# Optimization experiments

Measured on AMD Instinct MI355X. Metric: run time of the kernel, lower is better.

Reference implementation:

```python
import jax, jax.numpy as jnp
import numpy as np

B, S, D = 2, 2048, 1024
H, E = 16, 64  # n_head, d_head


def setup_inputs() -> dict:
    key = jax.random.key(0)
    ks = jax.random.split(key, 5)
    scale = 0.02
    return {
        "x": jax.random.normal(ks[0], (B, S, D), dtype=jnp.float32),
        "Wq": jax.random.normal(ks[1], (H, D, E), dtype=jnp.float32) * scale,
        "Wk": jax.random.normal(ks[2], (H, D, E), dtype=jnp.float32) * scale,
        "Wv": jax.random.normal(ks[3], (H, D, E), dtype=jnp.float32) * scale,
        "Wproj": jax.random.normal(ks[4], (D, D), dtype=jnp.float32) * scale,
    }


def reference(x, Wq, Wk, Wv, Wproj):
    # Batched equivalent of the per-head Python loop.
    q = jnp.einsum("bsd,hde->bhse", x, Wq)  # [B,H,S,E]
    k = jnp.einsum("bsd,hde->bhse", x, Wk)
    v = jnp.einsum("bsd,hde->bhse", x, Wv)
    scale = 1.0 / jnp.sqrt(jnp.asarray(E, dtype=x.dtype))
    scores = jnp.einsum("bhse,bhte->bhst", q, k) * scale  # [B,H,S,S]
    causal = jnp.tril(jnp.ones((S, S), dtype=bool))
    scores = jnp.where(causal, scores, jnp.asarray(-jnp.inf, dtype=scores.dtype))
    attn = jax.nn.softmax(scores, axis=-1)
    out = jnp.einsum("bhst,bhte->bhse", attn, v)  # [B,H,S,E]
    # concat heads along last dim (head h -> contiguous slice), then proj
    out = out.transpose(0, 2, 1, 3).reshape(B, S, H * E)
    return out @ Wproj.T  # nn.Linear: y = x W^T
```

## Files before the change

kernel.cpp:

```cpp
#include <hip/hip_runtime.h>
#include <hip/hip_bf16.h>

typedef __attribute__((ext_vector_type(8))) short short8;
typedef __attribute__((ext_vector_type(4))) short s16x4;
typedef __attribute__((ext_vector_type(4))) float f32x4;
typedef __hip_bfloat16 bf16;

#define NB 2
#define NS 2048
#define ND 1024
#define NH 16
#define NE 64

#define QSCALE 0.1803368867f

#define ASYNC16(g, l) __builtin_amdgcn_global_load_lds( \
    (const __attribute__((address_space(1))) void*)(g), \
    (__attribute__((address_space(3))) void*)(l), 16, 0, 0)

__device__ __forceinline__ unsigned short bf16b(float x) {
  __hip_bfloat16 h = __float2bfloat16(x);
  unsigned short u;
  __builtin_memcpy(&u, &h, 2);
  return u;
}

__global__ __launch_bounds__(256) void prep_all(const float* __restrict__ x,
                                                bf16* __restrict__ xb,
                                                const float* __restrict__ wp,
                                                bf16* __restrict__ wpb,
                                                const float* __restrict__ Wq,
                                                const float* __restrict__ Wk,
                                                const float* __restrict__ Wv,
                                                bf16* __restrict__ WT) {
  const int bid = blockIdx.x;
  const int tid = threadIdx.x;
  if (bid < 2560) {
    const float* src;
    bf16* dst;
    int i;
    if (bid < 2048) { src = x;  dst = xb;  i = (bid * 256 + tid) * 8; }
    else            { src = wp; dst = wpb; i = ((bid - 2048) * 256 + tid) * 8; }
    const float4 a = *(const float4*)(src + i);
    const float4 b = *(const float4*)(src + i + 4);
    *(ushort4*)(dst + i)     = make_ushort4(bf16b(a.x), bf16b(a.y), bf16b(a.z), bf16b(a.w));
    *(ushort4*)(dst + i + 4) = make_ushort4(bf16b(b.x), bf16b(b.y), bf16b(b.z), bf16b(b.w));
    return;
  }
  const int tb = bid - 2560;
  const int w = tb >> 8;
  const int xx = tb & 255;
  const float* W = (w == 0) ? Wq : ((w == 1) ? Wk : Wv);
  const int h = xx >> 4, kt = xx & 15;
  __shared__ bf16 tile[64][65];
#pragma unroll
  for (int i = 0; i < 16; ++i) {
    const int idx = i * 256 + tid, kl = idx >> 6, e = idx & 63;
    tile[kl][e] = __float2bfloat16(W[((size_t)h * ND + kt * 64 + kl) * NE + e]);
  }
  __syncthreads();
#pragma unroll
  for (int i = 0; i < 16; ++i) {
    const int idx = i * 256 + tid, el = idx >> 6, kl = idx & 63;
    WT[((size_t)w * NH * NE + h * NE + el) * ND + kt * 64 + kl] = tile[kl][el];
  }
}

__global__ __launch_bounds__(256) void qkv_gemm(const bf16* __restrict__ X,
                                                const bf16* __restrict__ WT,
                                                bf16* __restrict__ Qo,
                                                bf16* __restrict__ Ko,
                                                bf16* __restrict__ Vo) {
  const int w = blockIdx.z;
  const bf16* Bm = WT + (size_t)w * (NH * NE * ND);
  const int n0 = blockIdx.x * 128, m0 = blockIdx.y * 128;
  __shared__ __align__(16) bf16 As[2][128 * 32];
  __shared__ __align__(16) bf16 Bs[2][128 * 32];
  const int tid = threadIdx.x;
  const int lane = tid & 63, wid = tid >> 6;
  const int wm = wid >> 1, wn = wid & 1;
  const int g = lane >> 4, c = lane & 15;
  const int row4 = tid >> 2;
  const int kcs = ((tid & 3) ^ ((tid >> 3) & 3)) * 8;

  auto stage = [&](int buf, int k0) {
    ASYNC16(X + (size_t)(m0 + row4) * ND + k0 + kcs, As[buf] + wid * 512);
    ASYNC16(X + (size_t)(m0 + 64 + row4) * ND + k0 + kcs, As[buf] + 2048 + wid * 512);
    ASYNC16(Bm + (size_t)(n0 + row4) * ND + k0 + kcs, Bs[buf] + wid * 512);
    ASYNC16(Bm + (size_t)(n0 + 64 + row4) * ND + k0 + kcs, Bs[buf] + 2048 + wid * 512);
  };

  f32x4 acc[4][4] = {};
  stage(0, 0);
  __syncthreads();
  int cur = 0;
  for (int k0 = 0; k0 < ND; k0 += 32) {
    if (k0 + 32 < ND) stage(cur ^ 1, k0 + 32);
    const short* as = (const short*)As[cur];
    const short* bs = (const short*)Bs[cur];
    short8 af[4], bq[4];
#pragma unroll
    for (int i = 0; i < 4; ++i)
      af[i] = *(const short8*)&as[(wm * 64 + i * 16 + c) * 32 + ((g ^ ((c >> 1) & 3)) * 8)];
#pragma unroll
    for (int j = 0; j < 4; ++j)
      bq[j] = *(const short8*)&bs[(wn * 64 + j * 16 + c) * 32 + ((g ^ ((c >> 1) & 3)) * 8)];
    __builtin_amdgcn_s_setprio(1);
#pragma unroll
    for (int i = 0; i < 4; ++i)
#pragma unroll
      for (int j = 0; j < 4; ++j)
        acc[i][j] = __builtin_amdgcn_mfma_f32_16x16x32_bf16(af[i], bq[j], acc[i][j], 0, 0, 0);
    __builtin_amdgcn_s_setprio(0);
    __syncthreads();
    cur ^= 1;
  }
  const float osc = (w == 0) ? QSCALE : 1.0f;
#pragma unroll
  for (int i = 0; i < 4; ++i) {
    const int mg0 = m0 + wm * 64 + i * 16 + g * 4;
#pragma unroll
    for (int j = 0; j < 4; ++j) {
      const int ng = n0 + wn * 64 + j * 16 + c;
      const int h = ng >> 6, e = ng & 63;
      if (w == 2) {
        const int b = mg0 >> 11, s = mg0 & 2047;
        ushort4 pk = make_ushort4(bf16b(acc[i][j][0]), bf16b(acc[i][j][1]),
                                  bf16b(acc[i][j][2]), bf16b(acc[i][j][3]));
        *(ushort4*)&Vo[(((size_t)b * NH + h) * NE + e) * NS + s] = pk;
      } else {
        bf16* O = (w == 0) ? Qo : Ko;
#pragma unroll
        for (int r = 0; r < 4; ++r) {
          const int m = mg0 + r, b = m >> 11, s = m & 2047;
          O[(((size_t)b * NH + h) * NS + s) * NE + e] = __float2bfloat16(acc[i][j][r] * osc);
        }
      }
    }
  }
}

__global__ __launch_bounds__(256, 4) void attn_fwd(const bf16* __restrict__ Qb,
                                                   const bf16* __restrict__ Kb,
                                                   const bf16* __restrict__ Vt,
                                                   bf16* __restrict__ AO) {
  const int bh = blockIdx.x;
  const int qi = blockIdx.y;
  const int a = qi & 7, k = qi >> 3;
  const int qt = (k == 0) ? a : (k == 1) ? 31 - a : (k == 2) ? a + 8 : 23 - a;
  const int q0 = qt * 64;
  __shared__ __align__(16) bf16 Ks[2][64 * 64];
  __shared__ __align__(16) bf16 Vs[2][64 * 64];
  __shared__ __align__(16) bf16 Ps[4][16 * 64];
  const int tid = threadIdx.x, lane = tid & 63, wid = tid >> 6;
  const int g = lane >> 4, c = lane & 15;
  const int sw8 = ((tid & 7) ^ ((tid >> 3) & 7)) * 8;
  const bf16* Qg = Qb + (size_t)bh * NS * NE;
  const bf16* Kg = Kb + (size_t)bh * NS * NE;
  const bf16* Vg = Vt + (size_t)bh * NE * NS;

  short8 aq[2];
#pragma unroll
  for (int kk = 0; kk < 2; ++kk)
    aq[kk] = *(const short8*)&Qg[(size_t)(q0 + wid * 16 + c) * NE + kk * 32 + g * 8];

  const short8 bones = {0x3F80, 0x3F80, 0x3F80, 0x3F80, 0x3F80, 0x3F80, 0x3F80, 0x3F80};

  f32x4 acc_o[4] = {};
  f32x4 acc_l = {};
  float mrun = -1.0e30f;

  auto stage = [&](int buf, int t0) {
    ASYNC16(Kg + (size_t)(t0 + (tid >> 3)) * NE + sw8,      Ks[buf] + wid * 512);
    ASYNC16(Kg + (size_t)(t0 + 32 + (tid >> 3)) * NE + sw8, Ks[buf] + 2048 + wid * 512);
    ASYNC16(Vg + (size_t)(tid >> 3) * NS + t0 + sw8,        Vs[buf] + wid * 512);
    ASYNC16(Vg + (size_t)(32 + (tid >> 3)) * NS + t0 + sw8, Vs[buf] + 2048 + wid * 512);
  };

  const int nt = qt + 1;
  int cur = 0;
  stage(0, 0);
  __syncthreads();
  for (int tt = 0; tt < nt; ++tt) {
    const int t0 = tt * 64;
    if (tt + 1 < nt) stage(cur ^ 1, t0 + 64);
    const bool diag = (tt == nt - 1);
    f32x4 sacc[4] = {};
    const short* ks = (const short*)Ks[cur];
    const short* vs = (const short*)Vs[cur];
    __builtin_amdgcn_s_setprio(1);
#pragma unroll
    for (int kk = 0; kk < 2; ++kk) {
      short8 bk[4];
#pragma unroll
      for (int tn = 0; tn < 4; ++tn)
        bk[tn] = *(const short8*)&ks[(tn * 16 + c) * 64 + (((kk * 4 + g) ^ (c & 7)) * 8)];
#pragma unroll
      for (int tn = 0; tn < 4; ++tn)
        sacc[tn] = __builtin_amdgcn_mfma_f32_16x16x32_bf16(bk[tn], aq[kk], sacc[tn], 0, 0, 0);
    }
    __builtin_amdgcn_s_setprio(0);
    float mx = -1.0e30f;
#pragma unroll
    for (int tn = 0; tn < 4; ++tn) {
#pragma unroll
      for (int r = 0; r < 4; ++r) {
        float v = sacc[tn][r];
        if (diag) {
          const int tcol = t0 + tn * 16 + g * 4 + r;
          const int qrow = q0 + wid * 16 + c;
          v = (tcol <= qrow) ? v : -1.0e30f;
          sacc[tn][r] = v;
        }
        mx = fmaxf(mx, v);
      }
    }
    if (__any(mx > mrun + 8.0f)) {
      mx = fmaxf(mx, __shfl_xor(mx, 16));
      mx = fmaxf(mx, __shfl_xor(mx, 32));
      const float mnew = fmaxf(mrun, mx);
      const float alpha = __builtin_exp2f(mrun - mnew);
      mrun = mnew;
      float al[4];
#pragma unroll
      for (int r = 0; r < 4; ++r) al[r] = __shfl(alpha, g * 4 + r);
#pragma unroll
      for (int fe = 0; fe < 4; ++fe)
#pragma unroll
        for (int r = 0; r < 4; ++r) acc_o[fe][r] *= al[r];
#pragma unroll
      for (int r = 0; r < 4; ++r) acc_l[r] *= al[r];
    }
    short* psw = (short*)Ps[wid];
#pragma unroll
    for (int tn = 0; tn < 4; ++tn) {
      s16x4 pw;
#pragma unroll
      for (int r = 0; r < 4; ++r)
        pw[r] = (short)bf16b(__builtin_exp2f(sacc[tn][r] - mrun));
      const int blk = (2 * tn + (g >> 1)) ^ (c & 7);
      *(s16x4*)&psw[c * 64 + blk * 8 + (g & 1) * 4] = pw;
    }
    const short* ps = (const short*)Ps[wid];
    __builtin_amdgcn_s_setprio(1);
#pragma unroll
    for (int ks2 = 0; ks2 < 2; ++ks2) {
      short8 ap, bv[4];
      ap = *(const short8*)&ps[c * 64 + (((ks2 * 4 + g) ^ (c & 7)) * 8)];
      acc_l = __builtin_amdgcn_mfma_f32_16x16x32_bf16(ap, bones, acc_l, 0, 0, 0);
#pragma unroll
      for (int fe = 0; fe < 4; ++fe)
        bv[fe] = *(const short8*)&vs[(fe * 16 + c) * 64 + (((ks2 * 4 + g) ^ (c & 7)) * 8)];
#pragma unroll
      for (int fe = 0; fe < 4; ++fe)
        acc_o[fe] = __builtin_amdgcn_mfma_f32_16x16x32_bf16(ap, bv[fe], acc_o[fe], 0, 0, 0);
    }
    __builtin_amdgcn_s_setprio(0);
    __syncthreads();
    cur ^= 1;
  }
  const int b = bh >> 4, h = bh & 15;
#pragma unroll
  for (int fe = 0; fe < 4; ++fe)
#pragma unroll
    for (int r = 0; r < 4; ++r) {
      const int s = q0 + wid * 16 + g * 4 + r;
      const float val = acc_o[fe][r] / acc_l[r];
      AO[((size_t)b * NS + s) * ND + h * NE + fe * 16 + c] = __float2bfloat16(val);
    }
}

__global__ __launch_bounds__(256) void proj_gemm(const bf16* __restrict__ A,
                                                 const bf16* __restrict__ Wp,
                                                 float* __restrict__ Y) {
  const int n0 = blockIdx.x * 128, m0 = blockIdx.y * 128;
  __shared__ __align__(16) bf16 As[2][128 * 32];
  __shared__ __align__(16) bf16 Bs[2][128 * 32];
  const int tid = threadIdx.x;
  const int lane = tid & 63, wid = tid >> 6;
  const int wm = wid >> 1, wn = wid & 1;
  const int g = lane >> 4, c = lane & 15;
  const int row4 = tid >> 2;
  const int kcs = ((tid & 3) ^ ((tid >> 3) & 3)) * 8;

  auto stage = [&](int buf, int k0) {
    ASYNC16(A + (size_t)(m0 + row4) * ND + k0 + kcs, As[buf] + wid * 512);
    ASYNC16(A + (size_t)(m0 + 64 + row4) * ND + k0 + kcs, As[buf] + 2048 + wid * 512);
    ASYNC16(Wp + (size_t)(n0 + row4) * ND + k0 + kcs, Bs[buf] + wid * 512);
    ASYNC16(Wp + (size_t)(n0 + 64 + row4) * ND + k0 + kcs, Bs[buf] + 2048 + wid * 512);
  };

  f32x4 acc[4][4] = {};
  stage(0, 0);
  __syncthreads();
  int cur = 0;
  for (int k0 = 0; k0 < ND; k0 += 32) {
    if (k0 + 32 < ND) stage(cur ^ 1, k0 + 32);
    const short* as = (const short*)As[cur];
    const short* bs = (const short*)Bs[cur];
    short8 af[4], bq[4];
#pragma unroll
    for (int i = 0; i < 4; ++i)
      af[i] = *(const short8*)&as[(wm * 64 + i * 16 + c) * 32 + ((g ^ ((c >> 1) & 3)) * 8)];
#pragma unroll
    for (int j = 0; j < 4; ++j)
      bq[j] = *(const short8*)&bs[(wn * 64 + j * 16 + c) * 32 + ((g ^ ((c >> 1) & 3)) * 8)];
    __builtin_amdgcn_s_setprio(1);
#pragma unroll
    for (int i = 0; i < 4; ++i)
#pragma unroll
      for (int j = 0; j < 4; ++j)
        acc[i][j] = __builtin_amdgcn_mfma_f32_16x16x32_bf16(af[i], bq[j], acc[i][j], 0, 0, 0);
    __builtin_amdgcn_s_setprio(0);
    __syncthreads();
    cur ^= 1;
  }
#pragma unroll
  for (int i = 0; i < 4; ++i) {
    const int mg0 = m0 + wm * 64 + i * 16 + g * 4;
#pragma unroll
    for (int j = 0; j < 4; ++j) {
      const int ng = n0 + wn * 64 + j * 16 + c;
#pragma unroll
      for (int r = 0; r < 4; ++r)
        Y[(size_t)(mg0 + r) * ND + ng] = acc[i][j][r];
    }
  }
}

extern "C" void kernel_launch(void* const* d_in, const int* in_sizes, int n_in,
                              void* d_out, int out_size, void* d_ws, size_t ws_size,
                              hipStream_t stream) {
  const float* x  = (const float*)d_in[0];
  const float* Wq = (const float*)d_in[1];
  const float* Wk = (const float*)d_in[2];
  const float* Wv = (const float*)d_in[3];
  const float* Wp = (const float*)d_in[4];
  float* out = (float*)d_out;

  bf16* ws = (bf16*)d_ws;
  bf16* Xb  = ws;
  bf16* WT  = Xb + (size_t)NB * NS * ND;
  bf16* Wpb = WT + (size_t)3 * NH * NE * ND;
  bf16* Qb  = Wpb + (size_t)ND * ND;
  bf16* Kb  = Qb + (size_t)NB * NH * NS * NE;
  bf16* Vt  = Kb + (size_t)NB * NH * NS * NE;
  bf16* AO  = Vt + (size_t)NB * NH * NS * NE;

  hipLaunchKernelGGL(prep_all, dim3(3328), dim3(256), 0, stream,
                     x, Xb, Wp, Wpb, Wq, Wk, Wv, WT);
  hipLaunchKernelGGL(qkv_gemm, dim3(8, 32, 3), dim3(256), 0, stream, Xb, WT, Qb, Kb, Vt);
  hipLaunchKernelGGL(attn_fwd, dim3(32, 32), dim3(256), 0, stream, Qb, Kb, Vt, AO);
  hipLaunchKernelGGL(proj_gemm, dim3(8, 32), dim3(256), 0, stream, AO, Wpb, out);
}
```

Baseline: 107.8 us.

## Process two 64-row query tiles per attention block to reuse K/V tiles

Each attention workgroup now handles 128 query rows as two 64-row sub-tiles that share every staged K/V tile. K fragments are loaded from LDS once and used for both sub-tiles, and the launch grid is halved. This cuts the global-to-LDS traffic and staging for K/V. In exchange it needs more registers (occupancy hint lowered from 4 to 2), there are fewer blocks to balance the causal workload, and the two sub-tiles are processed one after the other, sharing the P buffer.

After: 134.0 us. 24.3% more time.

```diff
diff --git a/kernel.cpp b/kernel.cpp
--- a/kernel.cpp
+++ b/kernel.cpp
@@ -140,15 +140,14 @@
   }
 }
 
-__global__ __launch_bounds__(256, 4) void attn_fwd(const bf16* __restrict__ Qb,
+__global__ __launch_bounds__(256, 2) void attn_fwd(const bf16* __restrict__ Qb,
                                                    const bf16* __restrict__ Kb,
                                                    const bf16* __restrict__ Vt,
                                                    bf16* __restrict__ AO) {
   const int bh = blockIdx.x;
-  const int qi = blockIdx.y;
-  const int a = qi & 7, k = qi >> 3;
-  const int qt = (k == 0) ? a : (k == 1) ? 31 - a : (k == 2) ? a + 8 : 23 - a;
-  const int q0 = qt * 64;
+  const int jj = blockIdx.y;
+  const int qt = (jj < 8) ? jj : 23 - jj;
+  const int q0 = qt * 128;
   __shared__ __align__(16) bf16 Ks[2][64 * 64];
   __shared__ __align__(16) bf16 Vs[2][64 * 64];
   __shared__ __align__(16) bf16 Ps[4][16 * 64];
@@ -158,17 +157,20 @@
   const bf16* Qg = Qb + (size_t)bh * NS * NE;
   const bf16* Kg = Kb + (size_t)bh * NS * NE;
   const bf16* Vg = Vt + (size_t)bh * NE * NS;
-
-  short8 aq[2];
-#pragma unroll
-  for (int kk = 0; kk < 2; ++kk)
-    aq[kk] = *(const short8*)&Qg[(size_t)(q0 + wid * 16 + c) * NE + kk * 32 + g * 8];
+  const int b = bh >> 4, h = bh & 15;
 
   const short8 bones = {0x3F80, 0x3F80, 0x3F80, 0x3F80, 0x3F80, 0x3F80, 0x3F80, 0x3F80};
 
-  f32x4 acc_o[4] = {};
-  f32x4 acc_l = {};
-  float mrun = -1.0e30f;
+  short8 aq[2][2];
+#pragma unroll
+  for (int qm = 0; qm < 2; ++qm)
+#pragma unroll
+    for (int kk = 0; kk < 2; ++kk)
+      aq[qm][kk] = *(const short8*)&Qg[(size_t)(q0 + 64 * qm + wid * 16 + c) * NE + kk * 32 + g * 8];
+
+  f32x4 acc_o[2][4] = {};
+  f32x4 acc_l[2] = {};
+  float mrun[2] = {-1.0e30f, -1.0e30f};
 
   auto stage = [&](int buf, int t0) {
     ASYNC16(Kg + (size_t)(t0 + (tid >> 3)) * NE + sw8,      Ks[buf] + wid * 512);
@@ -177,97 +179,105 @@
     ASYNC16(Vg + (size_t)(32 + (tid >> 3)) * NS + t0 + sw8, Vs[buf] + 2048 + wid * 512);
   };
 
-  const int nt = qt + 1;
+  const int nt = 2 * qt + 2;
   int cur = 0;
   stage(0, 0);
   __syncthreads();
   for (int tt = 0; tt < nt; ++tt) {
     const int t0 = tt * 64;
     if (tt + 1 < nt) stage(cur ^ 1, t0 + 64);
-    const bool diag = (tt == nt - 1);
-    f32x4 sacc[4] = {};
     const short* ks = (const short*)Ks[cur];
     const short* vs = (const short*)Vs[cur];
+    short8 bk[2][4];
     __builtin_amdgcn_s_setprio(1);
 #pragma unroll
-    for (int kk = 0; kk < 2; ++kk) {
-      short8 bk[4];
+    for (int kk = 0; kk < 2; ++kk)
 #pragma unroll
       for (int tn = 0; tn < 4; ++tn)
-        bk[tn] = *(const short8*)&ks[(tn * 16 + c) * 64 + (((kk * 4 + g) ^ (c & 7)) * 8)];
-#pragma unroll
-      for (int tn = 0; tn < 4; ++tn)
-        sacc[tn] = __builtin_amdgcn_mfma_f32_16x16x32_bf16(bk[tn], aq[kk], sacc[tn], 0, 0, 0);
+        bk[kk][tn] = *(const short8*)&ks[(tn * 16 + c) * 64 + (((kk * 4 + g) ^ (c & 7)) * 8)];
+    __builtin_amdgcn_s_setprio(0);
+#pragma unroll
+    for (int qm = 0; qm < 2; ++qm) {
+      if (qm == 0 && tt == nt - 1) continue;
+      const bool diag = (tt >= nt - 2 + qm);
+      f32x4 sacc[4] = {};
+      __builtin_amdgcn_s_setprio(1);
+#pragma unroll
+      for (int kk = 0; kk < 2; ++kk)
+#pragma unroll
+        for (int tn = 0; tn < 4; ++tn)
+          sacc[tn] = __builtin_amdgcn_mfma_f32_16x16x32_bf16(bk[kk][tn], aq[qm][kk], sacc[tn], 0, 0, 0);
+      __builtin_amdgcn_s_setprio(0);
+      float mx = -1.0e30f;
+#pragma unroll
+      for (int tn = 0; tn < 4; ++tn) {
+#pragma unroll
+        for (int r = 0; r < 4; ++r) {
+          float v = sacc[tn][r];
+          if (diag) {
+            const int tcol = t0 + tn * 16 + g * 4 + r;
+            const int qrow = q0 + 64 * qm + wid * 16 + c;
+            v = (tcol <= qrow) ? v : -1.0e30f;
+            sacc[tn][r] = v;
+          }
+          mx = fmaxf(mx, v);
+        }
+      }
+      if (__any(mx > mrun[qm] + 8.0f)) {
+        mx = fmaxf(mx, __shfl_xor(mx, 16));
+        mx = fmaxf(mx, __shfl_xor(mx, 32));
+        const float mnew = fmaxf(mrun[qm], mx);
+        const float alpha = __builtin_exp2f(mrun[qm] - mnew);
+        mrun[qm] = mnew;
+        float al[4];
+#pragma unroll
+        for (int r = 0; r < 4; ++r) al[r] = __shfl(alpha, g * 4 + r);
+#pragma unroll
+        for (int fe = 0; fe < 4; ++fe)
+#pragma unroll
+          for (int r = 0; r < 4; ++r) acc_o[qm][fe][r] *= al[r];
+#pragma unroll
+        for (int r = 0; r < 4; ++r) acc_l[qm][r] *= al[r];
+      }
+      short* psw = (short*)Ps[wid];
+#pragma unroll
+      for (int tn = 0; tn < 4; ++tn) {
+        s16x4 pw;
+#pragma unroll
+        for (int r = 0; r < 4; ++r)
+          pw[r] = (short)bf16b(__builtin_exp2f(sacc[tn][r] - mrun[qm]));
+        const int blk = (2 * tn + (g >> 1)) ^ (c & 7);
+        *(s16x4*)&psw[c * 64 + blk * 8 + (g & 1) * 4] = pw;
+      }
+      const short* ps = (const short*)Ps[wid];
+      __builtin_amdgcn_s_setprio(1);
+#pragma unroll
+      for (int ks2 = 0; ks2 < 2; ++ks2) {
+        short8 ap, bv[4];
+        ap = *(const short8*)&ps[c * 64 + (((ks2 * 4 + g) ^ (c & 7)) * 8)];
+        acc_l[qm] = __builtin_amdgcn_mfma_f32_16x16x32_bf16(ap, bones, acc_l[qm], 0, 0, 0);
+#pragma unroll
+        for (int fe = 0; fe < 4; ++fe)
+          bv[fe] = *(const short8*)&vs[(fe * 16 + c) * 64 + (((ks2 * 4 + g) ^ (c & 7)) * 8)];
+#pragma unroll
+        for (int fe = 0; fe < 4; ++fe)
+          acc_o[qm][fe] = __builtin_amdgcn_mfma_f32_16x16x32_bf16(ap, bv[fe], acc_o[qm][fe], 0, 0, 0);
+      }
+      __builtin_amdgcn_s_setprio(0);
     }
-    __builtin_amdgcn_s_setprio(0);
-    float mx = -1.0e30f;
-#pragma unroll
-    for (int tn = 0; tn < 4; ++tn) {
-#pragma unroll
-      for (int r = 0; r < 4; ++r) {
-        float v = sacc[tn][r];
-        if (diag) {
-          const int tcol = t0 + tn * 16 + g * 4 + r;
-          const int qrow = q0 + wid * 16 + c;
-          v = (tcol <= qrow) ? v : -1.0e30f;
-          sacc[tn][r] = v;
-        }
-        mx = fmaxf(mx, v);
-      }
-    }
-    if (__any(mx > mrun + 8.0f)) {
-      mx = fmaxf(mx, __shfl_xor(mx, 16));
-      mx = fmaxf(mx, __shfl_xor(mx, 32));
-      const float mnew = fmaxf(mrun, mx);
-      const float alpha = __builtin_exp2f(mrun - mnew);
-      mrun = mnew;
-      float al[4];
-#pragma unroll
-      for (int r = 0; r < 4; ++r) al[r] = __shfl(alpha, g * 4 + r);
-#pragma unroll
-      for (int fe = 0; fe < 4; ++fe)
-#pragma unroll
-        for (int r = 0; r < 4; ++r) acc_o[fe][r] *= al[r];
-#pragma unroll
-      for (int r = 0; r < 4; ++r) acc_l[r] *= al[r];
-    }
-    short* psw = (short*)Ps[wid];
-#pragma unroll
-    for (int tn = 0; tn < 4; ++tn) {
-      s16x4 pw;
-#pragma unroll
-      for (int r = 0; r < 4; ++r)
-        pw[r] = (short)bf16b(__builtin_exp2f(sacc[tn][r] - mrun));
-      const int blk = (2 * tn + (g >> 1)) ^ (c & 7);
-      *(s16x4*)&psw[c * 64 + blk * 8 + (g & 1) * 4] = pw;
-    }
-    const short* ps = (const short*)Ps[wid];
-    __builtin_amdgcn_s_setprio(1);
-#pragma unroll
-    for (int ks2 = 0; ks2 < 2; ++ks2) {
-      short8 ap, bv[4];
-      ap = *(const short8*)&ps[c * 64 + (((ks2 * 4 + g) ^ (c & 7)) * 8)];
-      acc_l = __builtin_amdgcn_mfma_f32_16x16x32_bf16(ap, bones, acc_l, 0, 0, 0);
-#pragma unroll
-      for (int fe = 0; fe < 4; ++fe)
-        bv[fe] = *(const short8*)&vs[(fe * 16 + c) * 64 + (((ks2 * 4 + g) ^ (c & 7)) * 8)];
-#pragma unroll
-      for (int fe = 0; fe < 4; ++fe)
-        acc_o[fe] = __builtin_amdgcn_mfma_f32_16x16x32_bf16(ap, bv[fe], acc_o[fe], 0, 0, 0);
-    }
-    __builtin_amdgcn_s_setprio(0);
     __syncthreads();
     cur ^= 1;
   }
-  const int b = bh >> 4, h = bh & 15;
-#pragma unroll
-  for (int fe = 0; fe < 4; ++fe)
-#pragma unroll
-    for (int r = 0; r < 4; ++r) {
-      const int s = q0 + wid * 16 + g * 4 + r;
-      const float val = acc_o[fe][r] / acc_l[r];
-      AO[((size_t)b * NS + s) * ND + h * NE + fe * 16 + c] = __float2bfloat16(val);
-    }
+#pragma unroll
+  for (int qm = 0; qm < 2; ++qm)
+#pragma unroll
+    for (int fe = 0; fe < 4; ++fe)
+#pragma unroll
+      for (int r = 0; r < 4; ++r) {
+        const int s = q0 + 64 * qm + wid * 16 + g * 4 + r;
+        const float val = acc_o[qm][fe][r] / acc_l[qm][r];
+        AO[((size_t)b * NS + s) * ND + h * NE + fe * 16 + c] = __float2bfloat16(val);
+      }
 }
 
 __global__ __launch_bounds__(256) void proj_gemm(const bf16* __restrict__ A,
@@ -350,6 +360,6 @@
   hipLaunchKernelGGL(prep_all, dim3(3328), dim3(256), 0, stream,
                      x, Xb, Wp, Wpb, Wq, Wk, Wv, WT);
   hipLaunchKernelGGL(qkv_gemm, dim3(8, 32, 3), dim3(256), 0, stream, Xb, WT, Qb, Kb, Vt);
-  hipLaunchKernelGGL(attn_fwd, dim3(32, 32), dim3(256), 0, stream, Qb, Kb, Vt, AO);
+  hipLaunchKernelGGL(attn_fwd, dim3(32, 16), dim3(256), 0, stream, Qb, Kb, Vt, AO);
   hipLaunchKernelGGL(proj_gemm, dim3(8, 32), dim3(256), 0, stream, AO, Wpb, out);
 }
```
